# Kernel optimization log

Measured on AMD Instinct MI355X. Metric: run time of the kernel, lower is better.

## Reference

```python
import jax, jax.numpy as jnp
import numpy as np

G, T, E = 20000, 2, 4        # n_genes, n_tech, n_expansion
U = G * T                    # independent tiny-linear units
N_ETH = 4                    # ethnicity cardinality (interaction index stride)
DNN_DIMS = [20038, 5009, 1252, 313, 78, 2]  # shrinkage_factor=4, min=64, final=2


def setup_inputs() -> dict:
    key = jax.random.key(0)
    ks = jax.random.split(key, 24)
    B = 512
    inp = {
        "expression": jax.random.normal(ks[0], (B, T, G), jnp.float32),
        "clinical_categorical": jax.random.randint(ks[1], (B, 3), 0, 4),
        "clinical_non_categorical": jax.random.normal(ks[2], (B, 2, 10), jnp.float32),
        # ParallelBellowsLayers params
        "bw1": 0.05 * jax.random.normal(ks[3], (U, E), jnp.float32),
        "bb1": 0.05 * jax.random.normal(ks[4], (U, E), jnp.float32),
        "bw2": 0.05 * jax.random.normal(ks[5], (U, E), jnp.float32),
        "bb2": 0.05 * jax.random.normal(ks[6], (U,), jnp.float32),
        # ParallelGeneLayers params
        "gw": 0.05 * jax.random.normal(ks[7], (G, T), jnp.float32),
        "gb": 0.05 * jax.random.normal(ks[8], (G,), jnp.float32),
        # embeddings
        "race_emb": 0.05 * jax.random.normal(ks[9], (10, 8), jnp.float32),
        "eth_emb": 0.05 * jax.random.normal(ks[10], (4, 4), jnp.float32),
        "inter_emb": 0.05 * jax.random.normal(ks[11], (40, 8), jnp.float32),
        "prot_emb": 0.05 * jax.random.normal(ks[12], (20, 8), jnp.float32),
        # ClinicalMissingMask params (n_variables=10)
        "mask_w": 0.05 * jax.random.normal(ks[13], (10, 2), jnp.float32),
        "mask_b": 0.05 * jax.random.normal(ks[14], (10,), jnp.float32),
    }
    for i in range(5):
        din, dout = DNN_DIMS[i], DNN_DIMS[i + 1]
        inp[f"dnn_w{i}"] = (jax.random.normal(ks[15 + i], (din, dout), jnp.float32)
                             / jnp.sqrt(jnp.float32(din)))
        inp[f"dnn_b{i}"] = jnp.zeros((dout,), jnp.float32)
    return inp


def _forward(expression, clinical_categorical, clinical_non_categorical,
             bw1, bb1, bw2, bb2, gw, gb,
             race_emb, eth_emb, inter_emb, prot_emb, mask_w, mask_b,
             dnn_w0, dnn_b0, dnn_w1, dnn_b1, dnn_w2, dnn_b2,
             dnn_w3, dnn_b3, dnn_w4, dnn_b4):
    B = expression.shape[0]
    # --- CombinedGeneModel ---
    # bellows: per-unit 1->E->1 linear; units are tech-major (view(B,T,G))
    xf = expression.reshape(B, U)                              # [B, U]
    h = jax.nn.relu(xf[:, :, None] * bw1[None] + bb1[None])    # [B, U, E]
    s = jax.nn.relu(jnp.einsum('bue,ue->bu', h, bw2) + bb2)    # [B, U]
    # per-gene combine over tech
    s3 = s.reshape(B, T, G)
    expr = jax.nn.relu(jnp.einsum('btg,gt->bg', s3, gw) + gb)  # [B, G]
    # --- ClinicalModel ---
    cc = clinical_categorical
    race = race_emb[cc[:, 0]]
    eth = eth_emb[cc[:, 1]]
    inter = inter_emb[cc[:, 0] * N_ETH + cc[:, 1]]
    prot = prot_emb[cc[:, 2]]
    nc = jax.nn.relu(jnp.einsum('bcv,vc->bv', clinical_non_categorical, mask_w)
                     + mask_b)                                 # [B, 10]
    clin = jnp.concatenate([race, eth, inter, prot, nc], axis=1)
    # --- ConnectedLayers (shrinking MLP) ---
    x = jnp.concatenate([expr, clin], axis=1)                  # [B, 20038]
    for w, b in [(dnn_w0, dnn_b0), (dnn_w1, dnn_b1),
                 (dnn_w2, dnn_b2), (dnn_w3, dnn_b3)]:
        x = jax.nn.relu(x @ w + b)
    return x @ dnn_w4 + dnn_b4                                 # [B, 2]


def reference(expression, clinical_categorical, clinical_non_categorical,
              bw1, bb1, bw2, bb2, gw, gb,
              race_emb, eth_emb, inter_emb, prot_emb, mask_w, mask_b,
              dnn_w0, dnn_b0, dnn_w1, dnn_b1, dnn_w2, dnn_b2,
              dnn_w3, dnn_b3, dnn_w4, dnn_b4):
    return _forward(expression, clinical_categorical, clinical_non_categorical,
                    bw1, bb1, bw2, bb2, gw, gb,
                    race_emb, eth_emb, inter_emb, prot_emb, mask_w, mask_b,
                    dnn_w0, dnn_b0, dnn_w1, dnn_b1, dnn_w2, dnn_b2,
                    dnn_w3, dnn_b3, dnn_w4, dnn_b4)
```

## Files before the change

kernel.cpp:

```cpp
#include <hip/hip_runtime.h>
#include <hip/hip_bf16.h>

typedef __attribute__((ext_vector_type(8))) short bf16x8;
typedef __attribute__((ext_vector_type(4))) float f32x4;
typedef __attribute__((ext_vector_type(4))) int   i32x4;
typedef __attribute__((ext_vector_type(4))) unsigned short u16x4;
typedef unsigned short u16;

#define G_ 20000
#define B_ 512

__device__ __forceinline__ u16 f2bf(float x) {
  __hip_bfloat16 h = __float2bfloat16(x);
  return __builtin_bit_cast(u16, h);
}
__device__ __forceinline__ float bf2f(u16 u) {
  unsigned int v = ((unsigned int)u) << 16;
  return __builtin_bit_cast(float, v);
}

__device__ __forceinline__ void glds16(const void* g, void* l) {
  __builtin_amdgcn_global_load_lds(
      (const __attribute__((address_space(1))) void*)g,
      (__attribute__((address_space(3))) void*)l, 16, 0, 0);
}

__device__ __forceinline__ int swz(int b, int kk) {
  return b * 64 + ((((kk >> 3) & 7) ^ (b & 7)) << 3) + (kk & 7);
}

__global__ void k_gene(const float* __restrict__ expr,
                       const float* __restrict__ bw1, const float* __restrict__ bb1,
                       const float* __restrict__ bw2, const float* __restrict__ bb2,
                       const float* __restrict__ gw,  const float* __restrict__ gb,
                       const int* __restrict__ cc, const float* __restrict__ cnc,
                       const float* __restrict__ race, const float* __restrict__ eth,
                       const float* __restrict__ inter, const float* __restrict__ prot,
                       const float* __restrict__ mw, const float* __restrict__ mb,
                       u16* __restrict__ Xt) {
  int b0 = blockIdx.y * 32;

  if (blockIdx.x == 79) {
    int b = b0 + (threadIdx.x >> 3);
    int j0 = (threadIdx.x & 7) * 12;
    int c0 = cc[b * 3], c1 = cc[b * 3 + 1], c2 = cc[b * 3 + 2];
    float nc[10];
    #pragma unroll
    for (int v = 0; v < 10; ++v)
      nc[v] = fmaxf(cnc[b * 20 + v] * mw[v * 2] + cnc[b * 20 + 10 + v] * mw[v * 2 + 1] + mb[v], 0.f);
    #pragma unroll
    for (int jj = 0; jj < 12; ++jj) {
      int j = j0 + jj;
      float v;
      if (j < 8)       v = race[c0 * 8 + j];
      else if (j < 12) v = eth[c1 * 4 + (j - 8)];
      else if (j < 20) v = inter[(c0 * 4 + c1) * 8 + (j - 12)];
      else if (j < 28) v = prot[c2 * 8 + (j - 20)];
      else if (j < 38) v = nc[j - 28];
      else             v = 0.f;
      int k = 20000 + j;
      Xt[(size_t)(k >> 6) * 32768 + swz(b, k & 63)] = f2bf(v);
    }
    return;
  }

  int g = blockIdx.x * 256 + threadIdx.x;
  if (g >= G_) return;

  f32x4 w1a = ((const f32x4*)bw1)[g];
  f32x4 w1b = ((const f32x4*)bw1)[G_ + g];
  f32x4 b1a = ((const f32x4*)bb1)[g];
  f32x4 b1b = ((const f32x4*)bb1)[G_ + g];
  f32x4 w2a = ((const f32x4*)bw2)[g];
  f32x4 w2b = ((const f32x4*)bw2)[G_ + g];
  float bb2a = bb2[g], bb2b = bb2[G_ + g];
  float gw0 = gw[g * 2], gw1 = gw[g * 2 + 1];
  float gbg = gb[g];

  u16* slab = Xt + (size_t)(g >> 6) * 32768;
  int kk = g & 63, ch = (kk >> 3) & 7, klo = kk & 7;

  #pragma unroll 4
  for (int b = b0; b < b0 + 32; ++b) {
    float x0 = expr[(size_t)(b * 2) * G_ + g];
    float x1 = expr[(size_t)(b * 2 + 1) * G_ + g];
    float h0 = fmaxf(x0 * w1a.x + b1a.x, 0.f);
    float h1 = fmaxf(x0 * w1a.y + b1a.y, 0.f);
    float h2 = fmaxf(x0 * w1a.z + b1a.z, 0.f);
    float h3 = fmaxf(x0 * w1a.w + b1a.w, 0.f);
    float s0 = fmaxf(h0 * w2a.x + h1 * w2a.y + h2 * w2a.z + h3 * w2a.w + bb2a, 0.f);
    float g0 = fmaxf(x1 * w1b.x + b1b.x, 0.f);
    float g1 = fmaxf(x1 * w1b.y + b1b.y, 0.f);
    float g2 = fmaxf(x1 * w1b.z + b1b.z, 0.f);
    float g3 = fmaxf(x1 * w1b.w + b1b.w, 0.f);
    float s1 = fmaxf(g0 * w2b.x + g1 * w2b.y + g2 * w2b.z + g3 * w2b.w + bb2b, 0.f);
    float e = fmaxf(s0 * gw0 + s1 * gw1 + gbg, 0.f);
    slab[b * 64 + ((ch ^ (b & 7)) << 3) + klo] = f2bf(e);
  }
}

__global__ __launch_bounds__(512, 2) void k_gemm(
    const u16* __restrict__ Xt, const float* __restrict__ W,
    float* __restrict__ part, int nSlabs, int Kvalid, int Nvalid, int Npad) {
  __shared__ __align__(16) u16 As[2][512 * 64];
  __shared__ __align__(16) u16 Bs[128 * 64];

  const int tid = threadIdx.x;
  const int nt = blockIdx.x, split = blockIdx.y, S = gridDim.y;
  const int n0 = nt * 128;
  const int s0 = (int)(((long)split * nSlabs) / S);
  const int s1 = (int)(((long)(split + 1) * nSlabs) / S);
  const int sLast = s1 - 1;

  const int lane = tid & 63, wv = tid >> 6;
  const int wr = wv >> 1, wc = wv & 1;
  const int l15 = lane & 15, l4 = lane >> 4;
  const int bn = tid & 127, bh = tid >> 7;
  const int nW = n0 + bn;
  const bool nok = nW < Nvalid;

  f32x4 acc[8][4];
  #pragma unroll
  for (int i = 0; i < 8; ++i)
    #pragma unroll
    for (int j = 0; j < 4; ++j)
      acc[i][j] = f32x4{0.f, 0.f, 0.f, 0.f};

  float wreg[16];

  auto GLDS = [&](int s, int buf) {
    const char* sb = (const char*)(Xt + (size_t)s * 32768);
    char* lb = (char*)&As[buf][0];
    #pragma unroll
    for (int j = 0; j < 8; ++j) {
      int q = wv * 8 + j;
      glds16(sb + q * 1024 + lane * 16, lb + q * 1024);
    }
  };
  auto WLOAD = [&](int s) {
    int kb = s * 64 + bh * 16;
    #pragma unroll
    for (int j = 0; j < 16; ++j) {
      int k = kb + j;
      wreg[j] = (nok && k < Kvalid) ? W[(size_t)k * Nvalid + nW] : 0.f;
    }
  };
  auto BSTORE = [&]() {
    #pragma unroll
    for (int h = 0; h < 2; ++h) {
      i32x4 pk;
      #pragma unroll
      for (int q = 0; q < 4; ++q) {
        u16 lo = f2bf(wreg[h * 8 + q * 2]);
        u16 hi = f2bf(wreg[h * 8 + q * 2 + 1]);
        pk[q] = (int)(unsigned)lo | ((int)(unsigned)hi << 16);
      }
      int cch = bh * 2 + h;
      *(i32x4*)&Bs[bn * 64 + ((cch ^ (bn & 7)) << 3)] = pk;
    }
  };
  auto COMPUTE = [&](int buf) {
    #pragma unroll
    for (int kk = 0; kk < 2; ++kk) {
      bf16x8 bfr[4];
      #pragma unroll
      for (int nf = 0; nf < 4; ++nf) {
        int n = wc * 64 + nf * 16 + l15;
        int cch = kk * 4 + l4;
        bfr[nf] = *(const bf16x8*)&Bs[n * 64 + ((cch ^ (n & 7)) << 3)];
      }
      #pragma unroll
      for (int mf = 0; mf < 8; ++mf) {
        int m = wr * 128 + mf * 16 + l15;
        int cch = kk * 4 + l4;
        bf16x8 af = *(const bf16x8*)&As[buf][m * 64 + ((cch ^ (m & 7)) << 3)];
        #pragma unroll
        for (int nf = 0; nf < 4; ++nf)
          acc[mf][nf] = __builtin_amdgcn_mfma_f32_16x16x32_bf16(af, bfr[nf], acc[mf][nf], 0, 0, 0);
      }
    }
  };

  GLDS(s0, 0); WLOAD(s0);
  asm volatile("s_waitcnt vmcnt(0)" ::: "memory");
  BSTORE();
  int sp1 = (s0 + 1 > sLast) ? sLast : s0 + 1;
  GLDS(sp1, 1); WLOAD(sp1);
  asm volatile("s_waitcnt lgkmcnt(0)" ::: "memory");
  __builtin_amdgcn_s_barrier();
  __builtin_amdgcn_sched_barrier(0);

  int c = 0;
  for (int s = s0; s < s1; ++s) {
    COMPUTE(c);
    __builtin_amdgcn_s_barrier();
    __builtin_amdgcn_sched_barrier(0);
    int sp = (s + 2 > sLast) ? sLast : s + 2;
    GLDS(sp, c);
    asm volatile("s_waitcnt vmcnt(8)" ::: "memory");
    BSTORE();
    WLOAD(sp);
    asm volatile("s_waitcnt lgkmcnt(0)" ::: "memory");
    __builtin_amdgcn_s_barrier();
    __builtin_amdgcn_sched_barrier(0);
    c ^= 1;
  }

  float* outp = part + (size_t)split * B_ * Npad;
  #pragma unroll
  for (int mf = 0; mf < 8; ++mf)
    #pragma unroll
    for (int nf = 0; nf < 4; ++nf) {
      int col = n0 + wc * 64 + nf * 16 + l15;
      int rb = wr * 128 + mf * 16 + l4 * 4;
      #pragma unroll
      for (int r = 0; r < 4; ++r)
        outp[(size_t)(rb + r) * Npad + col] = acc[mf][nf][r];
    }
}

__global__ void k_reduce(const float* __restrict__ part, const float* __restrict__ bias,
                         u16* __restrict__ Ht, int S, int Npad, int Nout, int Nvalid) {
  int idx = blockIdx.x * 256 + threadIdx.x;
  int perRow = Nout >> 2;
  if (idx >= B_ * perRow) return;
  int b = idx / perRow;
  int n = (idx - b * perRow) * 4;
  float v[4] = {0.f, 0.f, 0.f, 0.f};
  for (int s = 0; s < S; ++s) {
    const f32x4 p = *(const f32x4*)&part[(size_t)s * B_ * Npad + (size_t)b * Npad + n];
    #pragma unroll
    for (int r = 0; r < 4; ++r) v[r] += p[r];
  }
  u16x4 o;
  #pragma unroll
  for (int r = 0; r < 4; ++r) {
    float bi = (n + r < Nvalid) ? bias[n + r] : 0.f;
    o[r] = f2bf(fmaxf(v[r] + bi, 0.f));
  }
  *(u16x4*)&Ht[(size_t)(n >> 6) * 32768 + swz(b, n & 63)] = o;
}

__global__ void k_tail(const u16* __restrict__ H3t,
                       const float* __restrict__ W3, const float* __restrict__ b3,
                       const float* __restrict__ W4, const float* __restrict__ b4,
                       float* __restrict__ out) {
  __shared__ float h3[320];
  __shared__ float h4[80];
  int b = blockIdx.x, tid = threadIdx.x;
  for (int i = tid; i < 313; i += 128)
    h3[i] = bf2f(H3t[(size_t)(i >> 6) * 32768 + swz(b, i & 63)]);
  __syncthreads();
  if (tid < 78) {
    float a = b3[tid];
    #pragma unroll 4
    for (int k = 0; k < 313; ++k) a += h3[k] * W3[k * 78 + tid];
    h4[tid] = fmaxf(a, 0.f);
  }
  __syncthreads();
  if (tid < 2) {
    float a = b4[tid];
    for (int k = 0; k < 78; ++k) a += h4[k] * W4[k * 2 + tid];
    out[b * 2 + tid] = a;
  }
}

extern "C" void kernel_launch(void* const* d_in, const int* in_sizes, int n_in,
                              void* d_out, int out_size, void* d_ws, size_t ws_size,
                              hipStream_t stream) {
  const float* expr = (const float*)d_in[0];
  const int*   cc   = (const int*)d_in[1];
  const float* cnc  = (const float*)d_in[2];
  const float* bw1  = (const float*)d_in[3];
  const float* bb1  = (const float*)d_in[4];
  const float* bw2  = (const float*)d_in[5];
  const float* bb2  = (const float*)d_in[6];
  const float* gw   = (const float*)d_in[7];
  const float* gb   = (const float*)d_in[8];
  const float* race = (const float*)d_in[9];
  const float* eth  = (const float*)d_in[10];
  const float* inter= (const float*)d_in[11];
  const float* prot = (const float*)d_in[12];
  const float* mw   = (const float*)d_in[13];
  const float* mb   = (const float*)d_in[14];
  const float* w0 = (const float*)d_in[15]; const float* b0 = (const float*)d_in[16];
  const float* w1 = (const float*)d_in[17]; const float* b1 = (const float*)d_in[18];
  const float* w2 = (const float*)d_in[19]; const float* b2 = (const float*)d_in[20];
  const float* w3 = (const float*)d_in[21]; const float* b3 = (const float*)d_in[22];
  const float* w4 = (const float*)d_in[23]; const float* b4 = (const float*)d_in[24];

  u16* Xt  = (u16*)d_ws;
  u16* H1t = Xt  + (size_t)314 * 32768;
  u16* H2t = H1t + (size_t)80 * 32768;
  u16* H3t = H2t + (size_t)20 * 32768;
  float* part = (float*)(H3t + (size_t)5 * 32768);

  k_gene<<<dim3(80, 16), 256, 0, stream>>>(expr, bw1, bb1, bw2, bb2, gw, gb,
                                           cc, cnc, race, eth, inter, prot, mw, mb, Xt);

  k_gemm<<<dim3(40, 6), 512, 0, stream>>>(Xt, w0, part, 314, 20038, 5009, 5120);
  k_reduce<<<2560, 256, 0, stream>>>(part, b0, H1t, 6, 5120, 5120, 5009);

  k_gemm<<<dim3(10, 12), 512, 0, stream>>>(H1t, w1, part, 80, 5009, 1252, 1280);
  k_reduce<<<640, 256, 0, stream>>>(part, b1, H2t, 12, 1280, 1280, 1252);

  k_gemm<<<dim3(3, 5), 512, 0, stream>>>(H2t, w2, part, 20, 1252, 313, 384);
  k_reduce<<<160, 256, 0, stream>>>(part, b2, H3t, 5, 384, 320, 313);

  k_tail<<<512, 128, 0, stream>>>(H3t, w3, b3, w4, b4, (float*)d_out);
}
```

Baseline: 336.1 us.

## Shrink GEMM N-tile to 64, single-buffer A, and fuse last reduce into tail

The GEMM kernel moves from 128-wide to 64-wide N tiles with a single A buffer. This cuts shared memory and registers so four blocks can be resident per CU, and the grids double in the N dimension. The software pipeline becomes a single-buffered load/compute sequence with fewer barriers. The third split-K reduce kernel is dropped: the tail kernel now sums the partials and applies bias and ReLU itself. In exchange, each weight tile is reused less, more A reloads happen per output, and load latency is less hidden behind compute.

```diff
diff --git a/kernel.cpp b/kernel.cpp
--- a/kernel.cpp
+++ b/kernel.cpp
@@ -99,38 +99,38 @@
   }
 }
 
-__global__ __launch_bounds__(512, 2) void k_gemm(
+__global__ __launch_bounds__(512, 4) void k_gemm(
     const u16* __restrict__ Xt, const float* __restrict__ W,
     float* __restrict__ part, int nSlabs, int Kvalid, int Nvalid, int Npad) {
-  __shared__ __align__(16) u16 As[2][512 * 64];
-  __shared__ __align__(16) u16 Bs[128 * 64];
+  __shared__ __align__(16) u16 As[512 * 64];
+  __shared__ __align__(16) u16 Bs[64 * 64];
 
   const int tid = threadIdx.x;
   const int nt = blockIdx.x, split = blockIdx.y, S = gridDim.y;
-  const int n0 = nt * 128;
+  const int n0 = nt * 64;
   const int s0 = (int)(((long)split * nSlabs) / S);
   const int s1 = (int)(((long)(split + 1) * nSlabs) / S);
   const int sLast = s1 - 1;
 
   const int lane = tid & 63, wv = tid >> 6;
-  const int wr = wv >> 1, wc = wv & 1;
   const int l15 = lane & 15, l4 = lane >> 4;
-  const int bn = tid & 127, bh = tid >> 7;
+  const int bn = lane;
+  const int bh = wv;
   const int nW = n0 + bn;
   const bool nok = nW < Nvalid;
 
-  f32x4 acc[8][4];
+  f32x4 acc[4][4];
   #pragma unroll
-  for (int i = 0; i < 8; ++i)
+  for (int i = 0; i < 4; ++i)
     #pragma unroll
     for (int j = 0; j < 4; ++j)
       acc[i][j] = f32x4{0.f, 0.f, 0.f, 0.f};
 
-  float wreg[16];
-
-  auto GLDS = [&](int s, int buf) {
+  float wreg[8];
+
+  auto GLDS = [&](int s) {
     const char* sb = (const char*)(Xt + (size_t)s * 32768);
-    char* lb = (char*)&As[buf][0];
+    char* lb = (char*)&As[0];
     #pragma unroll
     for (int j = 0; j < 8; ++j) {
       int q = wv * 8 + j;
@@ -138,42 +138,38 @@
     }
   };
   auto WLOAD = [&](int s) {
-    int kb = s * 64 + bh * 16;
-    #pragma unroll
-    for (int j = 0; j < 16; ++j) {
+    int kb = s * 64 + bh * 8;
+    #pragma unroll
+    for (int j = 0; j < 8; ++j) {
       int k = kb + j;
       wreg[j] = (nok && k < Kvalid) ? W[(size_t)k * Nvalid + nW] : 0.f;
     }
   };
   auto BSTORE = [&]() {
-    #pragma unroll
-    for (int h = 0; h < 2; ++h) {
-      i32x4 pk;
-      #pragma unroll
-      for (int q = 0; q < 4; ++q) {
-        u16 lo = f2bf(wreg[h * 8 + q * 2]);
-        u16 hi = f2bf(wreg[h * 8 + q * 2 + 1]);
-        pk[q] = (int)(unsigned)lo | ((int)(unsigned)hi << 16);
-      }
-      int cch = bh * 2 + h;
-      *(i32x4*)&Bs[bn * 64 + ((cch ^ (bn & 7)) << 3)] = pk;
-    }
+    i32x4 pk;
+    #pragma unroll
+    for (int q = 0; q < 4; ++q) {
+      u16 lo = f2bf(wreg[q * 2]);
+      u16 hi = f2bf(wreg[q * 2 + 1]);
+      pk[q] = (int)(unsigned)lo | ((int)(unsigned)hi << 16);
+    }
+    *(i32x4*)&Bs[bn * 64 + ((bh ^ (bn & 7)) << 3)] = pk;
   };
-  auto COMPUTE = [&](int buf) {
+  auto COMPUTE = [&]() {
     #pragma unroll
     for (int kk = 0; kk < 2; ++kk) {
       bf16x8 bfr[4];
       #pragma unroll
       for (int nf = 0; nf < 4; ++nf) {
-        int n = wc * 64 + nf * 16 + l15;
+        int n = nf * 16 + l15;
         int cch = kk * 4 + l4;
         bfr[nf] = *(const bf16x8*)&Bs[n * 64 + ((cch ^ (n & 7)) << 3)];
       }
       #pragma unroll
-      for (int mf = 0; mf < 8; ++mf) {
-        int m = wr * 128 + mf * 16 + l15;
+      for (int mf = 0; mf < 4; ++mf) {
+        int m = wv * 64 + mf * 16 + l15;
         int cch = kk * 4 + l4;
-        bf16x8 af = *(const bf16x8*)&As[buf][m * 64 + ((cch ^ (m & 7)) << 3)];
+        bf16x8 af = *(const bf16x8*)&As[m * 64 + ((cch ^ (m & 7)) << 3)];
         #pragma unroll
         for (int nf = 0; nf < 4; ++nf)
           acc[mf][nf] = __builtin_amdgcn_mfma_f32_16x16x32_bf16(af, bfr[nf], acc[mf][nf], 0, 0, 0);
@@ -181,38 +177,31 @@
     }
   };
 
-  GLDS(s0, 0); WLOAD(s0);
-  asm volatile("s_waitcnt vmcnt(0)" ::: "memory");
+  GLDS(s0); WLOAD(s0);
   BSTORE();
-  int sp1 = (s0 + 1 > sLast) ? sLast : s0 + 1;
-  GLDS(sp1, 1); WLOAD(sp1);
-  asm volatile("s_waitcnt lgkmcnt(0)" ::: "memory");
+  WLOAD((s0 + 1 > sLast) ? sLast : s0 + 1);
+  asm volatile("s_waitcnt vmcnt(8) lgkmcnt(0)" ::: "memory");
   __builtin_amdgcn_s_barrier();
-  __builtin_amdgcn_sched_barrier(0);
-
-  int c = 0;
+
   for (int s = s0; s < s1; ++s) {
-    COMPUTE(c);
+    COMPUTE();
     __builtin_amdgcn_s_barrier();
-    __builtin_amdgcn_sched_barrier(0);
-    int sp = (s + 2 > sLast) ? sLast : s + 2;
-    GLDS(sp, c);
-    asm volatile("s_waitcnt vmcnt(8)" ::: "memory");
-    BSTORE();
-    WLOAD(sp);
-    asm volatile("s_waitcnt lgkmcnt(0)" ::: "memory");
-    __builtin_amdgcn_s_barrier();
-    __builtin_amdgcn_sched_barrier(0);
-    c ^= 1;
+    if (s + 1 <= sLast) {
+      GLDS(s + 1);
+      BSTORE();
+      WLOAD((s + 2 > sLast) ? sLast : s + 2);
+      asm volatile("s_waitcnt vmcnt(8) lgkmcnt(0)" ::: "memory");
+      __builtin_amdgcn_s_barrier();
+    }
   }
 
   float* outp = part + (size_t)split * B_ * Npad;
   #pragma unroll
-  for (int mf = 0; mf < 8; ++mf)
+  for (int mf = 0; mf < 4; ++mf)
     #pragma unroll
     for (int nf = 0; nf < 4; ++nf) {
-      int col = n0 + wc * 64 + nf * 16 + l15;
-      int rb = wr * 128 + mf * 16 + l4 * 4;
+      int col = n0 + nf * 16 + l15;
+      int rb = wv * 64 + mf * 16 + l4 * 4;
       #pragma unroll
       for (int r = 0; r < 4; ++r)
         outp[(size_t)(rb + r) * Npad + col] = acc[mf][nf][r];
@@ -241,15 +230,20 @@
   *(u16x4*)&Ht[(size_t)(n >> 6) * 32768 + swz(b, n & 63)] = o;
 }
 
-__global__ void k_tail(const u16* __restrict__ H3t,
+__global__ void k_tail(const float* __restrict__ part2, const float* __restrict__ b2,
                        const float* __restrict__ W3, const float* __restrict__ b3,
                        const float* __restrict__ W4, const float* __restrict__ b4,
-                       float* __restrict__ out) {
+                       int S2, int Npad2, float* __restrict__ out) {
   __shared__ float h3[320];
   __shared__ float h4[80];
   int b = blockIdx.x, tid = threadIdx.x;
-  for (int i = tid; i < 313; i += 128)
-    h3[i] = bf2f(H3t[(size_t)(i >> 6) * 32768 + swz(b, i & 63)]);
+  for (int n = tid; n < 320; n += 128) {
+    float v = 0.f;
+    for (int s = 0; s < S2; ++s)
+      v += part2[(size_t)s * B_ * Npad2 + (size_t)b * Npad2 + n];
+    float bi = (n < 313) ? b2[n] : 0.f;
+    h3[n] = fmaxf(v + bi, 0.f);
+  }
   __syncthreads();
   if (tid < 78) {
     float a = b3[tid];
@@ -292,20 +286,18 @@
   u16* Xt  = (u16*)d_ws;
   u16* H1t = Xt  + (size_t)314 * 32768;
   u16* H2t = H1t + (size_t)80 * 32768;
-  u16* H3t = H2t + (size_t)20 * 32768;
-  float* part = (float*)(H3t + (size_t)5 * 32768);
+  float* part = (float*)(H2t + (size_t)20 * 32768);
 
   k_gene<<<dim3(80, 16), 256, 0, stream>>>(expr, bw1, bb1, bw2, bb2, gw, gb,
                                            cc, cnc, race, eth, inter, prot, mw, mb, Xt);
 
-  k_gemm<<<dim3(40, 6), 512, 0, stream>>>(Xt, w0, part, 314, 20038, 5009, 5120);
+  k_gemm<<<dim3(80, 6), 512, 0, stream>>>(Xt, w0, part, 314, 20038, 5009, 5120);
   k_reduce<<<2560, 256, 0, stream>>>(part, b0, H1t, 6, 5120, 5120, 5009);
 
-  k_gemm<<<dim3(10, 12), 512, 0, stream>>>(H1t, w1, part, 80, 5009, 1252, 1280);
-  k_reduce<<<640, 256, 0, stream>>>(part, b1, H2t, 12, 1280, 1280, 1252);
-
-  k_gemm<<<dim3(3, 5), 512, 0, stream>>>(H2t, w2, part, 20, 1252, 313, 384);
-  k_reduce<<<160, 256, 0, stream>>>(part, b2, H3t, 5, 384, 320, 313);
-
-  k_tail<<<512, 128, 0, stream>>>(H3t, w3, b3, w4, b4, (float*)d_out);
-}
+  k_gemm<<<dim3(20, 8), 512, 0, stream>>>(H1t, w1, part, 80, 5009, 1252, 1280);
+  k_reduce<<<640, 256, 0, stream>>>(part, b1, H2t, 8, 1280, 1280, 1252);
+
+  k_gemm<<<dim3(6, 5), 512, 0, stream>>>(H2t, w2, part, 20, 1252, 313, 384);
+
+  k_tail<<<512, 128, 0, stream>>>(part, b2, w3, b3, w4, b4, 5, 384, (float*)d_out);
+}
```

Result: faster. 319.5 us (-5.0%).

## Fuse all stages into one persistent kernel with grid barriers

Applied to the files above, without the earlier changes.

Replaces the gene, three GEMM, reduce and tail launches with a single persistent 256-block kernel that separates stages with atomic-counter grid barriers. The GEMM drops from a double-buffered A tile to a single buffer, and the second layer's split-K changes from 12 to 8. The tail now folds in the last reduce, so the H3 buffer is no longer written. This is meant to remove launch gaps and per-launch overhead. In exchange it adds spin-wait barriers, leaves many blocks idle during the smaller GEMMs, and loses A-tile prefetch overlap.

```diff
diff --git a/kernel.cpp b/kernel.cpp
--- a/kernel.cpp
+++ b/kernel.cpp
@@ -9,14 +9,11 @@
 
 #define G_ 20000
 #define B_ 512
+#define NBLK 256
 
 __device__ __forceinline__ u16 f2bf(float x) {
   __hip_bfloat16 h = __float2bfloat16(x);
   return __builtin_bit_cast(u16, h);
-}
-__device__ __forceinline__ float bf2f(u16 u) {
-  unsigned int v = ((unsigned int)u) << 16;
-  return __builtin_bit_cast(float, v);
 }
 
 __device__ __forceinline__ void glds16(const void* g, void* l) {
@@ -29,108 +26,45 @@
   return b * 64 + ((((kk >> 3) & 7) ^ (b & 7)) << 3) + (kk & 7);
 }
 
-__global__ void k_gene(const float* __restrict__ expr,
-                       const float* __restrict__ bw1, const float* __restrict__ bb1,
-                       const float* __restrict__ bw2, const float* __restrict__ bb2,
-                       const float* __restrict__ gw,  const float* __restrict__ gb,
-                       const int* __restrict__ cc, const float* __restrict__ cnc,
-                       const float* __restrict__ race, const float* __restrict__ eth,
-                       const float* __restrict__ inter, const float* __restrict__ prot,
-                       const float* __restrict__ mw, const float* __restrict__ mb,
-                       u16* __restrict__ Xt) {
-  int b0 = blockIdx.y * 32;
-
-  if (blockIdx.x == 79) {
-    int b = b0 + (threadIdx.x >> 3);
-    int j0 = (threadIdx.x & 7) * 12;
-    int c0 = cc[b * 3], c1 = cc[b * 3 + 1], c2 = cc[b * 3 + 2];
-    float nc[10];
-    #pragma unroll
-    for (int v = 0; v < 10; ++v)
-      nc[v] = fmaxf(cnc[b * 20 + v] * mw[v * 2] + cnc[b * 20 + 10 + v] * mw[v * 2 + 1] + mb[v], 0.f);
-    #pragma unroll
-    for (int jj = 0; jj < 12; ++jj) {
-      int j = j0 + jj;
-      float v;
-      if (j < 8)       v = race[c0 * 8 + j];
-      else if (j < 12) v = eth[c1 * 4 + (j - 8)];
-      else if (j < 20) v = inter[(c0 * 4 + c1) * 8 + (j - 12)];
-      else if (j < 28) v = prot[c2 * 8 + (j - 20)];
-      else if (j < 38) v = nc[j - 28];
-      else             v = 0.f;
-      int k = 20000 + j;
-      Xt[(size_t)(k >> 6) * 32768 + swz(b, k & 63)] = f2bf(v);
-    }
-    return;
-  }
-
-  int g = blockIdx.x * 256 + threadIdx.x;
-  if (g >= G_) return;
-
-  f32x4 w1a = ((const f32x4*)bw1)[g];
-  f32x4 w1b = ((const f32x4*)bw1)[G_ + g];
-  f32x4 b1a = ((const f32x4*)bb1)[g];
-  f32x4 b1b = ((const f32x4*)bb1)[G_ + g];
-  f32x4 w2a = ((const f32x4*)bw2)[g];
-  f32x4 w2b = ((const f32x4*)bw2)[G_ + g];
-  float bb2a = bb2[g], bb2b = bb2[G_ + g];
-  float gw0 = gw[g * 2], gw1 = gw[g * 2 + 1];
-  float gbg = gb[g];
-
-  u16* slab = Xt + (size_t)(g >> 6) * 32768;
-  int kk = g & 63, ch = (kk >> 3) & 7, klo = kk & 7;
-
-  #pragma unroll 4
-  for (int b = b0; b < b0 + 32; ++b) {
-    float x0 = expr[(size_t)(b * 2) * G_ + g];
-    float x1 = expr[(size_t)(b * 2 + 1) * G_ + g];
-    float h0 = fmaxf(x0 * w1a.x + b1a.x, 0.f);
-    float h1 = fmaxf(x0 * w1a.y + b1a.y, 0.f);
-    float h2 = fmaxf(x0 * w1a.z + b1a.z, 0.f);
-    float h3 = fmaxf(x0 * w1a.w + b1a.w, 0.f);
-    float s0 = fmaxf(h0 * w2a.x + h1 * w2a.y + h2 * w2a.z + h3 * w2a.w + bb2a, 0.f);
-    float g0 = fmaxf(x1 * w1b.x + b1b.x, 0.f);
-    float g1 = fmaxf(x1 * w1b.y + b1b.y, 0.f);
-    float g2 = fmaxf(x1 * w1b.z + b1b.z, 0.f);
-    float g3 = fmaxf(x1 * w1b.w + b1b.w, 0.f);
-    float s1 = fmaxf(g0 * w2b.x + g1 * w2b.y + g2 * w2b.z + g3 * w2b.w + bb2b, 0.f);
-    float e = fmaxf(s0 * gw0 + s1 * gw1 + gbg, 0.f);
-    slab[b * 64 + ((ch ^ (b & 7)) << 3) + klo] = f2bf(e);
-  }
-}
-
-__global__ __launch_bounds__(512, 2) void k_gemm(
-    const u16* __restrict__ Xt, const float* __restrict__ W,
-    float* __restrict__ part, int nSlabs, int Kvalid, int Nvalid, int Npad) {
-  __shared__ __align__(16) u16 As[2][512 * 64];
-  __shared__ __align__(16) u16 Bs[128 * 64];
-
-  const int tid = threadIdx.x;
-  const int nt = blockIdx.x, split = blockIdx.y, S = gridDim.y;
-  const int n0 = nt * 128;
+__global__ void k_zero(unsigned* cnt) {
+  if (threadIdx.x < 16) cnt[threadIdx.x] = 0;
+}
+
+__device__ __forceinline__ void gridbar(unsigned* cnt, int j) {
+  __syncthreads();
+  if (threadIdx.x == 0) {
+    __threadfence();
+    atomicAdd(&cnt[j], 1u);
+    while (atomicAdd(&cnt[j], 0u) < NBLK) __builtin_amdgcn_s_sleep(8);
+    __threadfence();
+  }
+  __syncthreads();
+}
+
+__device__ void gemm128(const u16* __restrict__ At, const float* __restrict__ W,
+                        float* __restrict__ part, u16* As, u16* Bs,
+                        int nSlabs, int S, int split, int nt,
+                        int Kvalid, int Nvalid, int Npad) {
+  const int tid = threadIdx.x, lane = tid & 63, wv = tid >> 6;
+  const int wr = wv >> 1, wc = wv & 1, l15 = lane & 15, l4 = lane >> 4;
+  const int bn = tid & 127, bh = tid >> 7;
+  const int n0 = nt * 128, nW = n0 + bn;
+  const bool nok = nW < Nvalid;
   const int s0 = (int)(((long)split * nSlabs) / S);
   const int s1 = (int)(((long)(split + 1) * nSlabs) / S);
   const int sLast = s1 - 1;
 
-  const int lane = tid & 63, wv = tid >> 6;
-  const int wr = wv >> 1, wc = wv & 1;
-  const int l15 = lane & 15, l4 = lane >> 4;
-  const int bn = tid & 127, bh = tid >> 7;
-  const int nW = n0 + bn;
-  const bool nok = nW < Nvalid;
-
   f32x4 acc[8][4];
   #pragma unroll
   for (int i = 0; i < 8; ++i)
     #pragma unroll
-    for (int j = 0; j < 4; ++j)
-      acc[i][j] = f32x4{0.f, 0.f, 0.f, 0.f};
+    for (int j = 0; j < 4; ++j) acc[i][j] = f32x4{0.f, 0.f, 0.f, 0.f};
 
   float wreg[16];
 
-  auto GLDS = [&](int s, int buf) {
-    const char* sb = (const char*)(Xt + (size_t)s * 32768);
-    char* lb = (char*)&As[buf][0];
+  auto GLDS = [&](int s) {
+    const char* sb = (const char*)(At + (size_t)s * 32768);
+    char* lb = (char*)As;
     #pragma unroll
     for (int j = 0; j < 8; ++j) {
       int q = wv * 8 + j;
@@ -159,7 +93,7 @@
       *(i32x4*)&Bs[bn * 64 + ((cch ^ (bn & 7)) << 3)] = pk;
     }
   };
-  auto COMPUTE = [&](int buf) {
+  auto COMPUTE = [&]() {
     #pragma unroll
     for (int kk = 0; kk < 2; ++kk) {
       bf16x8 bfr[4];
@@ -173,7 +107,7 @@
       for (int mf = 0; mf < 8; ++mf) {
         int m = wr * 128 + mf * 16 + l15;
         int cch = kk * 4 + l4;
-        bf16x8 af = *(const bf16x8*)&As[buf][m * 64 + ((cch ^ (m & 7)) << 3)];
+        bf16x8 af = *(const bf16x8*)&As[m * 64 + ((cch ^ (m & 7)) << 3)];
         #pragma unroll
         for (int nf = 0; nf < 4; ++nf)
           acc[mf][nf] = __builtin_amdgcn_mfma_f32_16x16x32_bf16(af, bfr[nf], acc[mf][nf], 0, 0, 0);
@@ -181,29 +115,23 @@
     }
   };
 
-  GLDS(s0, 0); WLOAD(s0);
-  asm volatile("s_waitcnt vmcnt(0)" ::: "memory");
+  WLOAD(s0);
   BSTORE();
-  int sp1 = (s0 + 1 > sLast) ? sLast : s0 + 1;
-  GLDS(sp1, 1); WLOAD(sp1);
-  asm volatile("s_waitcnt lgkmcnt(0)" ::: "memory");
+  GLDS(s0);
+  WLOAD((s0 + 1 > sLast) ? sLast : s0 + 1);
+  asm volatile("s_waitcnt vmcnt(16) lgkmcnt(0)" ::: "memory");
   __builtin_amdgcn_s_barrier();
-  __builtin_amdgcn_sched_barrier(0);
-
-  int c = 0;
+
   for (int s = s0; s < s1; ++s) {
-    COMPUTE(c);
+    COMPUTE();
     __builtin_amdgcn_s_barrier();
-    __builtin_amdgcn_sched_barrier(0);
-    int sp = (s + 2 > sLast) ? sLast : s + 2;
-    GLDS(sp, c);
-    asm volatile("s_waitcnt vmcnt(8)" ::: "memory");
-    BSTORE();
-    WLOAD(sp);
-    asm volatile("s_waitcnt lgkmcnt(0)" ::: "memory");
-    __builtin_amdgcn_s_barrier();
-    __builtin_amdgcn_sched_barrier(0);
-    c ^= 1;
+    if (s < sLast) {
+      BSTORE();
+      GLDS(s + 1);
+      WLOAD((s + 2 > sLast) ? sLast : s + 2);
+      asm volatile("s_waitcnt vmcnt(16) lgkmcnt(0)" ::: "memory");
+      __builtin_amdgcn_s_barrier();
+    }
   }
 
   float* outp = part + (size_t)split * B_ * Npad;
@@ -219,49 +147,164 @@
     }
 }
 
-__global__ void k_reduce(const float* __restrict__ part, const float* __restrict__ bias,
-                         u16* __restrict__ Ht, int S, int Npad, int Nout, int Nvalid) {
-  int idx = blockIdx.x * 256 + threadIdx.x;
-  int perRow = Nout >> 2;
-  if (idx >= B_ * perRow) return;
-  int b = idx / perRow;
-  int n = (idx - b * perRow) * 4;
-  float v[4] = {0.f, 0.f, 0.f, 0.f};
-  for (int s = 0; s < S; ++s) {
-    const f32x4 p = *(const f32x4*)&part[(size_t)s * B_ * Npad + (size_t)b * Npad + n];
-    #pragma unroll
-    for (int r = 0; r < 4; ++r) v[r] += p[r];
-  }
-  u16x4 o;
+__global__ __launch_bounds__(512, 2) void k_mega(
+    const float* __restrict__ expr, const int* __restrict__ cc,
+    const float* __restrict__ cnc,
+    const float* __restrict__ bw1, const float* __restrict__ bb1,
+    const float* __restrict__ bw2, const float* __restrict__ bb2,
+    const float* __restrict__ gw,  const float* __restrict__ gb,
+    const float* __restrict__ race, const float* __restrict__ eth,
+    const float* __restrict__ inter, const float* __restrict__ prot,
+    const float* __restrict__ mw, const float* __restrict__ mb,
+    const float* __restrict__ w0, const float* __restrict__ bias0,
+    const float* __restrict__ w1, const float* __restrict__ bias1,
+    const float* __restrict__ w2, const float* __restrict__ bias2,
+    const float* __restrict__ w3, const float* __restrict__ bias3,
+    const float* __restrict__ w4, const float* __restrict__ bias4,
+    u16* __restrict__ Xt, u16* __restrict__ H1t, u16* __restrict__ H2t,
+    float* __restrict__ part, unsigned* __restrict__ cnt,
+    float* __restrict__ out) {
+
+  __shared__ __align__(16) u16 As[512 * 64];
+  __shared__ __align__(16) u16 Bs[128 * 64];
+
+  const int tid = threadIdx.x, bid = blockIdx.x;
+
+  for (int w = bid; w < 656; w += NBLK) {
+    if (w < 640) {
+      int gc = w >> 4, bt = w & 15, bb = bt * 32;
+      int g = gc * 512 + tid;
+      if (g < G_) {
+        f32x4 w1a = ((const f32x4*)bw1)[g];
+        f32x4 w1b = ((const f32x4*)bw1)[G_ + g];
+        f32x4 b1a = ((const f32x4*)bb1)[g];
+        f32x4 b1b = ((const f32x4*)bb1)[G_ + g];
+        f32x4 w2a = ((const f32x4*)bw2)[g];
+        f32x4 w2b = ((const f32x4*)bw2)[G_ + g];
+        float bb2a = bb2[g], bb2b = bb2[G_ + g];
+        float gw0 = gw[g * 2], gw1 = gw[g * 2 + 1];
+        float gbg = gb[g];
+        u16* slab = Xt + (size_t)(g >> 6) * 32768;
+        int kk = g & 63, ch = (kk >> 3) & 7, klo = kk & 7;
+        #pragma unroll 4
+        for (int b = bb; b < bb + 32; ++b) {
+          float x0 = expr[(size_t)(b * 2) * G_ + g];
+          float x1 = expr[(size_t)(b * 2 + 1) * G_ + g];
+          float h0 = fmaxf(x0 * w1a.x + b1a.x, 0.f);
+          float h1 = fmaxf(x0 * w1a.y + b1a.y, 0.f);
+          float h2 = fmaxf(x0 * w1a.z + b1a.z, 0.f);
+          float h3 = fmaxf(x0 * w1a.w + b1a.w, 0.f);
+          float s0 = fmaxf(h0 * w2a.x + h1 * w2a.y + h2 * w2a.z + h3 * w2a.w + bb2a, 0.f);
+          float g0 = fmaxf(x1 * w1b.x + b1b.x, 0.f);
+          float g1 = fmaxf(x1 * w1b.y + b1b.y, 0.f);
+          float g2 = fmaxf(x1 * w1b.z + b1b.z, 0.f);
+          float g3 = fmaxf(x1 * w1b.w + b1b.w, 0.f);
+          float s1 = fmaxf(g0 * w2b.x + g1 * w2b.y + g2 * w2b.z + g3 * w2b.w + bb2b, 0.f);
+          float e = fmaxf(s0 * gw0 + s1 * gw1 + gbg, 0.f);
+          slab[b * 64 + ((ch ^ (b & 7)) << 3) + klo] = f2bf(e);
+        }
+      }
+    } else {
+      int bt = w - 640;
+      int b = bt * 32 + (tid >> 4);
+      int j0 = (tid & 15) * 6;
+      int c0 = cc[b * 3], c1 = cc[b * 3 + 1], c2 = cc[b * 3 + 2];
+      float nc[10];
+      #pragma unroll
+      for (int v = 0; v < 10; ++v)
+        nc[v] = fmaxf(cnc[b * 20 + v] * mw[v * 2] + cnc[b * 20 + 10 + v] * mw[v * 2 + 1] + mb[v], 0.f);
+      #pragma unroll
+      for (int jj = 0; jj < 6; ++jj) {
+        int j = j0 + jj;
+        float v;
+        if (j < 8)       v = race[c0 * 8 + j];
+        else if (j < 12) v = eth[c1 * 4 + (j - 8)];
+        else if (j < 20) v = inter[(c0 * 4 + c1) * 8 + (j - 12)];
+        else if (j < 28) v = prot[c2 * 8 + (j - 20)];
+        else if (j < 38) v = nc[j - 28];
+        else             v = 0.f;
+        int k = 20000 + j;
+        Xt[(size_t)(k >> 6) * 32768 + swz(b, k & 63)] = f2bf(v);
+      }
+    }
+  }
+  gridbar(cnt, 0);
+
+  if (bid < 240)
+    gemm128(Xt, w0, part, As, Bs, 314, 6, bid / 40, bid % 40, 20038, 5009, 5120);
+  gridbar(cnt, 1);
+
+  for (int u = bid * 512 + tid; u < 655360; u += NBLK * 512) {
+    int b = u / 1280, n = (u - b * 1280) * 4;
+    float v[4] = {0.f, 0.f, 0.f, 0.f};
+    #pragma unroll
+    for (int s = 0; s < 6; ++s) {
+      f32x4 p = *(const f32x4*)&part[(size_t)s * B_ * 5120 + (size_t)b * 5120 + n];
+      v[0] += p[0]; v[1] += p[1]; v[2] += p[2]; v[3] += p[3];
+    }
+    u16x4 o;
+    #pragma unroll
+    for (int r = 0; r < 4; ++r) {
+      float bi = (n + r < 5009) ? bias0[n + r] : 0.f;
+      o[r] = f2bf(fmaxf(v[r] + bi, 0.f));
+    }
+    *(u16x4*)&H1t[(size_t)(n >> 6) * 32768 + swz(b, n & 63)] = o;
+  }
+  gridbar(cnt, 2);
+
+  if (bid < 80)
+    gemm128(H1t, w1, part, As, Bs, 80, 8, bid / 10, bid % 10, 5009, 1252, 1280);
+  gridbar(cnt, 3);
+
+  for (int u = bid * 512 + tid; u < 163840; u += NBLK * 512) {
+    int b = u / 320, n = (u - b * 320) * 4;
+    float v[4] = {0.f, 0.f, 0.f, 0.f};
+    #pragma unroll
+    for (int s = 0; s < 8; ++s) {
+      f32x4 p = *(const f32x4*)&part[(size_t)s * B_ * 1280 + (size_t)b * 1280 + n];
+      v[0] += p[0]; v[1] += p[1]; v[2] += p[2]; v[3] += p[3];
+    }
+    u16x4 o;
+    #pragma unroll
+    for (int r = 0; r < 4; ++r) {
+      float bi = (n + r < 1252) ? bias1[n + r] : 0.f;
+      o[r] = f2bf(fmaxf(v[r] + bi, 0.f));
+    }
+    *(u16x4*)&H2t[(size_t)(n >> 6) * 32768 + swz(b, n & 63)] = o;
+  }
+  gridbar(cnt, 4);
+
+  if (bid < 15)
+    gemm128(H2t, w2, part, As, Bs, 20, 5, bid / 3, bid % 3, 1252, 313, 384);
+  gridbar(cnt, 5);
+
+  float* h3 = (float*)As;
+  float* h4 = h3 + 320;
   #pragma unroll
-  for (int r = 0; r < 4; ++r) {
-    float bi = (n + r < Nvalid) ? bias[n + r] : 0.f;
-    o[r] = f2bf(fmaxf(v[r] + bi, 0.f));
-  }
-  *(u16x4*)&Ht[(size_t)(n >> 6) * 32768 + swz(b, n & 63)] = o;
-}
-
-__global__ void k_tail(const u16* __restrict__ H3t,
-                       const float* __restrict__ W3, const float* __restrict__ b3,
-                       const float* __restrict__ W4, const float* __restrict__ b4,
-                       float* __restrict__ out) {
-  __shared__ float h3[320];
-  __shared__ float h4[80];
-  int b = blockIdx.x, tid = threadIdx.x;
-  for (int i = tid; i < 313; i += 128)
-    h3[i] = bf2f(H3t[(size_t)(i >> 6) * 32768 + swz(b, i & 63)]);
-  __syncthreads();
-  if (tid < 78) {
-    float a = b3[tid];
-    #pragma unroll 4
-    for (int k = 0; k < 313; ++k) a += h3[k] * W3[k * 78 + tid];
-    h4[tid] = fmaxf(a, 0.f);
-  }
-  __syncthreads();
-  if (tid < 2) {
-    float a = b4[tid];
-    for (int k = 0; k < 78; ++k) a += h4[k] * W4[k * 2 + tid];
-    out[b * 2 + tid] = a;
+  for (int rep = 0; rep < 2; ++rep) {
+    int r = bid * 2 + rep;
+    if (tid < 320) {
+      float v = 0.f;
+      #pragma unroll
+      for (int s = 0; s < 5; ++s)
+        v += part[(size_t)s * B_ * 384 + (size_t)r * 384 + tid];
+      float bi = (tid < 313) ? bias2[tid] : 0.f;
+      h3[tid] = fmaxf(v + bi, 0.f);
+    }
+    __syncthreads();
+    if (tid < 78) {
+      float a = bias3[tid];
+      #pragma unroll 4
+      for (int k = 0; k < 313; ++k) a += h3[k] * w3[k * 78 + tid];
+      h4[tid] = fmaxf(a, 0.f);
+    }
+    __syncthreads();
+    if (tid < 2) {
+      float a = bias4[tid];
+      for (int k = 0; k < 78; ++k) a += h4[k] * w4[k * 2 + tid];
+      out[r * 2 + tid] = a;
+    }
+    __syncthreads();
   }
 }
 
@@ -292,20 +335,12 @@
   u16* Xt  = (u16*)d_ws;
   u16* H1t = Xt  + (size_t)314 * 32768;
   u16* H2t = H1t + (size_t)80 * 32768;
-  u16* H3t = H2t + (size_t)20 * 32768;
-  float* part = (float*)(H3t + (size_t)5 * 32768);
-
-  k_gene<<<dim3(80, 16), 256, 0, stream>>>(expr, bw1, bb1, bw2, bb2, gw, gb,
-                                           cc, cnc, race, eth, inter, prot, mw, mb, Xt);
-
-  k_gemm<<<dim3(40, 6), 512, 0, stream>>>(Xt, w0, part, 314, 20038, 5009, 5120);
-  k_reduce<<<2560, 256, 0, stream>>>(part, b0, H1t, 6, 5120, 5120, 5009);
-
-  k_gemm<<<dim3(10, 12), 512, 0, stream>>>(H1t, w1, part, 80, 5009, 1252, 1280);
-  k_reduce<<<640, 256, 0, stream>>>(part, b1, H2t, 12, 1280, 1280, 1252);
-
-  k_gemm<<<dim3(3, 5), 512, 0, stream>>>(H2t, w2, part, 20, 1252, 313, 384);
-  k_reduce<<<160, 256, 0, stream>>>(part, b2, H3t, 5, 384, 320, 313);
-
-  k_tail<<<512, 128, 0, stream>>>(H3t, w3, b3, w4, b4, (float*)d_out);
-}
+  float* part = (float*)(H2t + (size_t)20 * 32768);
+  unsigned* cnt = (unsigned*)((char*)d_ws + (size_t)96 * 1024 * 1024);
+
+  k_zero<<<1, 64, 0, stream>>>(cnt);
+  k_mega<<<NBLK, 512, 0, stream>>>(expr, cc, cnc, bw1, bb1, bw2, bb2, gw, gb,
+                                   race, eth, inter, prot, mw, mb,
+                                   w0, b0, w1, b1, w2, b2, w3, b3, w4, b4,
+                                   Xt, H1t, H2t, part, cnt, (float*)d_out);
+}
```

After: 519.5 us. 1.55x slower.
